# Performance work log

Measured on AMD Instinct MI355X. Metric: run time of the kernel, lower is better.

The kernel has to match this reference:

```python
import jax, jax.numpy as jnp
import numpy as np

B, S, D, H = 4, 2048, 512, 8
HD = D // H  # head dim = 64


def setup_inputs() -> dict:
    key = jax.random.key(0)
    ks = jax.random.split(key, 7)
    s = 0.02
    return {
        "X": jax.random.normal(ks[0], (B, S, D), dtype=jnp.float32),
        "Y": jax.random.normal(ks[1], (B, S, D), dtype=jnp.float32),
        "Z": jax.random.normal(ks[2], (B, S, D), dtype=jnp.float32),
        # weights stored as [in, out] (torch Linear weight transposed)
        "Wq": jax.random.normal(ks[3], (D, D), dtype=jnp.float32) * s,
        "Wk": jax.random.normal(ks[4], (D, D), dtype=jnp.float32) * s,
        "Wv": jax.random.normal(ks[5], (D, D), dtype=jnp.float32) * s,  # dead in original forward
        "Wo": jax.random.normal(ks[6], (D, D), dtype=jnp.float32) * s,
    }


def _split_heads(t):
    # [B, S, D] -> [B, H, S, HD]
    return t.reshape(B, S, H, HD).transpose(0, 2, 1, 3)


def reference(X, Y, Z, Wq, Wk, Wv, Wo):
    q = _split_heads(X @ Wq)
    k = _split_heads(Y @ Wk)
    # NOTE: original module (faithfully) uses W_o for the value projection; W_v is unused.
    v = _split_heads(Z @ Wo)
    scores = jnp.einsum("bhqd,bhkd->bhqk", q, k) / jnp.sqrt(jnp.float32(HD))
    # sigmoid(s) > 0.5  <=>  s > 0 (sigmoid strictly monotone); keep score else 0
    scores = jnp.where(scores > 0, scores, jnp.float32(0))
    attn = jax.nn.softmax(scores, axis=-1)
    out = jnp.einsum("bhqk,bhkd->bhqd", attn, v)  # dropout inactive at eval
    out = out.transpose(0, 2, 1, 3).reshape(B, S, D)  # merge heads
    return out @ Wo
```

## Files before the change

kernel.cpp:

```cpp
#include <hip/hip_runtime.h>
#include <math.h>

#define S_LEN 2048
#define DIM   512
#define M_TOT 8192
#define NCH   (S_LEN / 64)

typedef __attribute__((ext_vector_type(8))) short bf16x8;
typedef __attribute__((ext_vector_type(4))) short bf16x4;
typedef __attribute__((ext_vector_type(4))) float f32x4;
typedef __attribute__((ext_vector_type(16))) float f32x16;

#define MFMA(a, b, c)   __builtin_amdgcn_mfma_f32_16x16x32_bf16((a), (b), (c), 0, 0, 0)
#define MFMA32(a, b, c) __builtin_amdgcn_mfma_f32_32x32x16_bf16((a), (b), (c), 0, 0, 0)

#define QSCALE 0.18033688011112042f

__device__ __forceinline__ short f2b(float x) {
    union { float f; unsigned u; } v; v.f = x;
    unsigned r = v.u + 0x7FFFu + ((v.u >> 16) & 1u);
    return (short)(r >> 16);
}

__device__ __forceinline__ unsigned cvtpk(float a, float b) {
    unsigned r;
    asm("v_cvt_pk_bf16_f32 %0, %1, %2" : "=v"(r) : "v"(a), "v"(b));
    return r;
}

__device__ __forceinline__ bf16x8 cvt8(float4 lo, float4 hi) {
    union { unsigned u[4]; bf16x8 v; } o;
    o.u[0] = cvtpk(lo.x, lo.y);
    o.u[1] = cvtpk(lo.z, lo.w);
    o.u[2] = cvtpk(hi.x, hi.y);
    o.u[3] = cvtpk(hi.z, hi.w);
    return o.v;
}

__device__ __forceinline__ float fast_exp2(float x) {
#if __has_builtin(__builtin_amdgcn_exp2f)
    return __builtin_amdgcn_exp2f(x);
#else
    return __expf(x * 0.693147180559945f);
#endif
}

__global__ __launch_bounds__(256) void prep_wt(const float* Wq, const float* Wk, const float* Wo,
                                               short* Wtq, short* Wtk, short* Wto) {
    const int zi = blockIdx.z;
    const float* W = zi == 0 ? Wq : zi == 1 ? Wk : Wo;
    short*      Wt = zi == 0 ? Wtq : zi == 1 ? Wtk : Wto;
    const float sc = zi == 0 ? QSCALE : 1.0f;
    __shared__ short Ts[64 * 72];
    const int t = threadIdx.x;
    const int k0 = blockIdx.x * 64, n0 = blockIdx.y * 64;
    #pragma unroll
    for (int it = 0; it < 4; ++it) {
        const int r = (t >> 4) + 16 * it;
        const int cq = t & 15;
        float4 v = *(const float4*)&W[(size_t)(k0 + r) * DIM + n0 + cq * 4];
        Ts[(4 * cq + 0) * 72 + r] = f2b(v.x * sc);
        Ts[(4 * cq + 1) * 72 + r] = f2b(v.y * sc);
        Ts[(4 * cq + 2) * 72 + r] = f2b(v.z * sc);
        Ts[(4 * cq + 3) * 72 + r] = f2b(v.w * sc);
    }
    __syncthreads();
    #pragma unroll
    for (int it = 0; it < 2; ++it) {
        const int n = (t >> 3) + 32 * it;
        const int sg = t & 7;
        *(bf16x8*)&Wt[(size_t)(n0 + n) * DIM + k0 + sg * 8] = *(const bf16x8*)&Ts[n * 72 + sg * 8];
    }
}

__global__ __launch_bounds__(256) void proj_gemm(const float* __restrict__ X,
                                                 const float* __restrict__ Y,
                                                 const float* __restrict__ Z,
                                                 const short* __restrict__ Wtq,
                                                 const short* __restrict__ Wtk,
                                                 const short* __restrict__ Wto,
                                                 short* __restrict__ Qb,
                                                 short* __restrict__ Kb,
                                                 short* __restrict__ Vt) {
    const int zi = blockIdx.y;
    const float* A  = zi == 0 ? X : zi == 1 ? Y : Z;
    const short* Bw = zi == 0 ? Wtq : zi == 1 ? Wtk : Wto;

    __shared__ short As[64 * 40];
    __shared__ short Bs[512 * 40];
    const int tid = threadIdx.x;
    const int w = tid >> 6, ln = tid & 63, l15 = ln & 15, quad = ln >> 4;
    const int m0 = blockIdx.x * 64;
    const int wn = w * 128;

    const int r0 = tid >> 2;
    const int sg = tid & 3;
    const float* ap = A + (size_t)(m0 + r0) * DIM + sg * 8;
    const short* bp = Bw + (size_t)r0 * DIM + sg * 8;

    float4 a0l = *(const float4*)ap, a0h = *(const float4*)(ap + 4);
    bf16x8 br[8];
    #pragma unroll
    for (int i = 0; i < 8; ++i)
        br[i] = *(const bf16x8*)(bp + (size_t)(64 * i) * DIM);

    f32x4 acc[4][8] = {};

    for (int k0 = 0; k0 < DIM; k0 += 32) {
        __syncthreads();
        *(bf16x8*)&As[r0 * 40 + sg * 8] = cvt8(a0l, a0h);
        #pragma unroll
        for (int i = 0; i < 8; ++i)
            *(bf16x8*)&Bs[(r0 + 64 * i) * 40 + sg * 8] = br[i];
        __syncthreads();
        const int kn = (k0 + 32 < DIM) ? k0 + 32 : 0;
        a0l = *(const float4*)(ap + kn); a0h = *(const float4*)(ap + kn + 4);
        #pragma unroll
        for (int i = 0; i < 8; ++i)
            br[i] = *(const bf16x8*)(bp + (size_t)(64 * i) * DIM + kn);

        bf16x8 af[4];
        #pragma unroll
        for (int mf = 0; mf < 4; ++mf)
            af[mf] = *(const bf16x8*)&As[(16 * mf + l15) * 40 + quad * 8];
        #pragma unroll
        for (int nf = 0; nf < 8; ++nf) {
            bf16x8 bfr = *(const bf16x8*)&Bs[(wn + 16 * nf + l15) * 40 + quad * 8];
            #pragma unroll
            for (int mf = 0; mf < 4; ++mf)
                acc[mf][nf] = MFMA(af[mf], bfr, acc[mf][nf]);
        }
    }

    if (zi < 2) {
        short* C = zi == 0 ? Qb : Kb;
        #pragma unroll
        for (int mf = 0; mf < 4; ++mf)
            #pragma unroll
            for (int nf = 0; nf < 8; ++nf)
                #pragma unroll
                for (int r = 0; r < 4; ++r)
                    C[(size_t)(m0 + 16 * mf + 4 * quad + r) * DIM + wn + 16 * nf + l15] =
                        f2b(acc[mf][nf][r]);
    } else {
        #pragma unroll
        for (int mf = 0; mf < 4; ++mf)
            #pragma unroll
            for (int nf = 0; nf < 8; ++nf) {
                const int col = wn + 16 * nf + l15;
                const int h = col >> 6, hd = col & 63;
                const int row0_ = m0 + 16 * mf + 4 * quad;
                const int bb = row0_ >> 11, s0 = row0_ & 2047;
                bf16x4 o = { f2b(acc[mf][nf][0]), f2b(acc[mf][nf][1]),
                             f2b(acc[mf][nf][2]), f2b(acc[mf][nf][3]) };
                *(bf16x4*)&Vt[((size_t)((bb * 8 + h) * 64 + hd)) * S_LEN + s0] = o;
            }
    }
}

__global__ __launch_bounds__(256) void out_gemm(const short* __restrict__ Ob,
                                                const short* __restrict__ Wto,
                                                float* __restrict__ Cout) {
    __shared__ short As[64 * 40];
    __shared__ short Bs[64 * 40];
    const int tid = threadIdx.x;
    const int w = tid >> 6, ln = tid & 63, l15 = ln & 15, quad = ln >> 4;

    const int f = blockIdx.x;
    const int swz = ((f & 7) << 7) | (f >> 3);
    const int m0 = (swz >> 3) * 64, n0 = (swz & 7) * 64;
    const int wm = (w & 1) * 32, wn = (w >> 1) * 32;

    const int row = tid >> 2;
    const int sg = tid & 3;
    const short* ap = Ob  + (size_t)(m0 + row) * DIM + sg * 8;
    const short* bp = Wto + (size_t)(n0 + row) * DIM + sg * 8;

    bf16x8 a0 = *(const bf16x8*)ap, b0 = *(const bf16x8*)bp;

    f32x4 acc[2][2] = {};

    for (int k0 = 0; k0 < DIM; k0 += 32) {
        __syncthreads();
        *(bf16x8*)&As[row * 40 + sg * 8] = a0;
        *(bf16x8*)&Bs[row * 40 + sg * 8] = b0;
        __syncthreads();
        const int kn = (k0 + 32 < DIM) ? k0 + 32 : 0;
        a0 = *(const bf16x8*)(ap + kn); b0 = *(const bf16x8*)(bp + kn);

        bf16x8 af[2], bf[2];
        #pragma unroll
        for (int mf = 0; mf < 2; ++mf) af[mf] = *(const bf16x8*)&As[(wm + 16 * mf + l15) * 40 + quad * 8];
        #pragma unroll
        for (int nf = 0; nf < 2; ++nf) bf[nf] = *(const bf16x8*)&Bs[(wn + 16 * nf + l15) * 40 + quad * 8];
        #pragma unroll
        for (int mf = 0; mf < 2; ++mf)
            #pragma unroll
            for (int nf = 0; nf < 2; ++nf)
                acc[mf][nf] = MFMA(af[mf], bf[nf], acc[mf][nf]);
    }
    #pragma unroll
    for (int mf = 0; mf < 2; ++mf)
        #pragma unroll
        for (int nf = 0; nf < 2; ++nf)
            #pragma unroll
            for (int r = 0; r < 4; ++r)
                Cout[(size_t)(m0 + wm + 16 * mf + 4 * quad + r) * DIM + n0 + wn + 16 * nf + l15] =
                    acc[mf][nf][r];
}

__global__ __launch_bounds__(256) void attn_mfma(const short* __restrict__ Qb,
                                                 const short* __restrict__ Kb,
                                                 const short* __restrict__ Vtg,
                                                 short* __restrict__ Ob) {
    __shared__ short Ks[2][64 * 72];
    __shared__ short Vs[2][64 * 72];
    __shared__ float Ds[4][32];

    const int tid = threadIdx.x;
    const int w = tid >> 6, ln = tid & 63, n31 = ln & 31, hL = ln >> 5;

    const int f = blockIdx.x;
    const int swz = ((f & 7) << 6) | (f >> 3);
    const int qt0 = (swz & 15) * 128;
    const int bh  = swz >> 4;
    const int b = bh >> 3, h = bh & 7;
    const size_t tokbase = (size_t)b * S_LEN;

    const int q0w = qt0 + 32 * w;
    bf16x8 qf[4];
    #pragma unroll
    for (int dk = 0; dk < 4; ++dk)
        qf[dk] = *(const bf16x8*)&Qb[(tokbase + q0w + n31) * DIM + h * 64 + 16 * dk + 8 * hL];

    const int srow = tid >> 2, sg = tid & 3;
    const short* kbase = Kb  + (tokbase + srow) * DIM + h * 64 + sg * 16;
    const short* vbase = Vtg + ((size_t)bh * 64 + srow) * S_LEN;

    union b8split { bf16x8 v; struct { bf16x4 lo, hi; } s; };

    bf16x8 kr0, kr1;
    b8split vrA, vrB;

    f32x16 oacc[2] = {};
    f32x4 d4 = {0.f, 0.f, 0.f, 0.f};

    kr0 = *(const bf16x8*)kbase;       kr1 = *(const bf16x8*)(kbase + 8);
    vrA.v = *(const bf16x8*)(vbase + 8 * sg);
    vrB.v = *(const bf16x8*)(vbase + 32 + 8 * sg);
    *(bf16x8*)&Ks[0][srow * 72 + sg * 16]     = kr0;
    *(bf16x8*)&Ks[0][srow * 72 + sg * 16 + 8] = kr1;
    {
        short* vrow = &Vs[0][srow * 72 + 16 * sg];
        *(bf16x4*)&vrow[0]  = vrA.s.lo;  *(bf16x4*)&vrow[8]  = vrA.s.hi;
        *(bf16x4*)&vrow[4]  = vrB.s.lo;  *(bf16x4*)&vrow[12] = vrB.s.hi;
    }
    kr0 = *(const bf16x8*)(kbase + (size_t)64 * DIM);
    kr1 = *(const bf16x8*)(kbase + (size_t)64 * DIM + 8);
    vrA.v = *(const bf16x8*)(vbase + 64 + 8 * sg);
    vrB.v = *(const bf16x8*)(vbase + 64 + 32 + 8 * sg);
    __syncthreads();

    for (int kc = 0; kc < NCH; ++kc) {
        const int cur = kc & 1;
        if (kc + 1 < NCH) {
            *(bf16x8*)&Ks[cur ^ 1][srow * 72 + sg * 16]     = kr0;
            *(bf16x8*)&Ks[cur ^ 1][srow * 72 + sg * 16 + 8] = kr1;
            short* vrow = &Vs[cur ^ 1][srow * 72 + 16 * sg];
            *(bf16x4*)&vrow[0]  = vrA.s.lo;  *(bf16x4*)&vrow[8]  = vrA.s.hi;
            *(bf16x4*)&vrow[4]  = vrB.s.lo;  *(bf16x4*)&vrow[12] = vrB.s.hi;
        }
        if (kc + 2 < NCH) {
            const size_t ko = (size_t)(kc + 2) * 64 * DIM;
            const size_t vo = (size_t)(kc + 2) * 64;
            kr0 = *(const bf16x8*)(kbase + ko);
            kr1 = *(const bf16x8*)(kbase + ko + 8);
            vrA.v = *(const bf16x8*)(vbase + vo + 8 * sg);
            vrB.v = *(const bf16x8*)(vbase + vo + 32 + 8 * sg);
        }

        f32x16 sacc[2] = {};
        __builtin_amdgcn_s_setprio(1);
        #pragma unroll
        for (int kt = 0; kt < 2; ++kt)
            #pragma unroll
            for (int dk = 0; dk < 4; ++dk) {
                bf16x8 ka = *(const bf16x8*)&Ks[cur][(32 * kt + n31) * 72 + 16 * dk + 8 * hL];
                sacc[kt] = MFMA32(ka, qf[dk], sacc[kt]);
            }
        __builtin_amdgcn_s_setprio(0);

        unsigned cp[16];
        #pragma unroll
        for (int kt = 0; kt < 2; ++kt)
            #pragma unroll
            for (int p = 0; p < 8; ++p) {
                const float e0 = fast_exp2(fmaxf(sacc[kt][2 * p], 0.f));
                const float e1 = fast_exp2(fmaxf(sacc[kt][2 * p + 1], 0.f));
                d4[p & 3] += e0 + e1;
                cp[8 * kt + p] = cvtpk(e0, e1);
            }

        __builtin_amdgcn_s_setprio(1);
        #pragma unroll
        for (int m = 0; m < 4; ++m) {
            union { unsigned u[4]; bf16x8 v; } pu;
            pu.u[0] = cp[2 * m];     pu.u[1] = cp[2 * m + 1];
            pu.u[2] = cp[2 * m + 8]; pu.u[3] = cp[2 * m + 9];
            #pragma unroll
            for (int nt = 0; nt < 2; ++nt) {
                bf16x8 vb = *(const bf16x8*)&Vs[cur][(32 * nt + n31) * 72 + 16 * m + 8 * hL];
                oacc[nt] = MFMA32(pu.v, vb, oacc[nt]);
            }
        }
        __builtin_amdgcn_s_setprio(0);
        __syncthreads();
    }

    float dtot = (d4[0] + d4[1]) + (d4[2] + d4[3]);
    dtot += __shfl_xor(dtot, 32);
    const float dinv = 1.0f / dtot;
    if (ln < 32) Ds[w][n31] = dinv;
    __syncthreads();
    f32x4 dv[4];
    #pragma unroll
    for (int g = 0; g < 4; ++g)
        dv[g] = *(const f32x4*)&Ds[w][8 * g + 4 * hL];

    #pragma unroll
    for (int nt = 0; nt < 2; ++nt)
        #pragma unroll
        for (int r = 0; r < 16; ++r) {
            const int qb = 32 * w + 4 * hL + 8 * (r >> 2) + (r & 3);
            Ob[(tokbase + qt0 + qb) * DIM + h * 64 + 32 * nt + n31] =
                f2b(oacc[nt][r] * dv[r >> 2][r & 3]);
        }
}

extern "C" void kernel_launch(void* const* d_in, const int* in_sizes, int n_in,
                              void* d_out, int out_size, void* d_ws, size_t ws_size,
                              hipStream_t stream) {
    const float* X  = (const float*)d_in[0];
    const float* Y  = (const float*)d_in[1];
    const float* Z  = (const float*)d_in[2];
    const float* Wq = (const float*)d_in[3];
    const float* Wk = (const float*)d_in[4];
    const float* Wo = (const float*)d_in[6];

    char* p = (char*)d_ws;
    const size_t MD = (size_t)M_TOT * DIM;
    short* Qb  = (short*)p; p += MD * 2;
    short* Kb  = (short*)p; p += MD * 2;
    short* Vt  = (short*)p; p += MD * 2;
    short* Ob  = (short*)p; p += MD * 2;
    short* Wtq = (short*)p; p += (size_t)DIM * DIM * 2;
    short* Wtk = (short*)p; p += (size_t)DIM * DIM * 2;
    short* Wto = (short*)p; p += (size_t)DIM * DIM * 2;

    prep_wt<<<dim3(8, 8, 3), 256, 0, stream>>>(Wq, Wk, Wo, Wtq, Wtk, Wto);
    proj_gemm<<<dim3(128, 3), 256, 0, stream>>>(X, Y, Z, Wtq, Wtk, Wto, Qb, Kb, Vt);
    attn_mfma<<<dim3(512), 256, 0, stream>>>(Qb, Kb, Vt, Ob);
    out_gemm<<<dim3(1024), 256, 0, stream>>>(Ob, Wto, (float*)d_out);
}
```

Measured before the change: 197.9 us.

## Retile projection GEMM to 64x128 tiles with 32x32 MFMA and swizzled grid

The projection GEMM now gives each block a 64x128 output tile instead of a full 64x512 row panel, which raises the grid from 384 to 1536 blocks and shrinks the B shared-memory tile fourfold. Inner math switches from 16x16x32 to 32x32x16 bf16 MFMA, so each wave owns a 64x32 slice held in two 16-float accumulators. The block index is swizzled so consecutive blocks share N tiles. The aim is better occupancy and CU coverage, at the cost of re-reading and re-converting the fp32 A rows four times and less reuse of A per load.

After: 193.5 us. 1.02x faster.

```diff
diff --git a/kernel.cpp b/kernel.cpp
--- a/kernel.cpp
+++ b/kernel.cpp
@@ -87,72 +87,68 @@
     const short* Bw = zi == 0 ? Wtq : zi == 1 ? Wtk : Wto;
 
     __shared__ short As[64 * 40];
-    __shared__ short Bs[512 * 40];
+    __shared__ short Bs[128 * 40];
     const int tid = threadIdx.x;
-    const int w = tid >> 6, ln = tid & 63, l15 = ln & 15, quad = ln >> 4;
-    const int m0 = blockIdx.x * 64;
-    const int wn = w * 128;
-
-    const int r0 = tid >> 2;
-    const int sg = tid & 3;
-    const float* ap = A + (size_t)(m0 + r0) * DIM + sg * 8;
-    const short* bp = Bw + (size_t)r0 * DIM + sg * 8;
+    const int w = tid >> 6, ln = tid & 63, n31 = ln & 31, hL = ln >> 5;
+
+    const int lin = blockIdx.x;
+    const int j = lin >> 3;
+    const int m0 = (((lin & 7) << 4) + (j >> 2)) * 64;
+    const int n0 = (j & 3) * 128;
+
+    const int row = tid >> 2;
+    const int sgk = (tid & 3) * 8;
+    const float* ap = A  + (size_t)(m0 + row) * DIM + sgk;
+    const short* bp = Bw + (size_t)(n0 + row) * DIM + sgk;
 
     float4 a0l = *(const float4*)ap, a0h = *(const float4*)(ap + 4);
-    bf16x8 br[8];
-    #pragma unroll
-    for (int i = 0; i < 8; ++i)
-        br[i] = *(const bf16x8*)(bp + (size_t)(64 * i) * DIM);
-
-    f32x4 acc[4][8] = {};
+    bf16x8 br0 = *(const bf16x8*)bp;
+    bf16x8 br1 = *(const bf16x8*)(bp + (size_t)64 * DIM);
+
+    f32x16 acc[2] = {};
 
     for (int k0 = 0; k0 < DIM; k0 += 32) {
         __syncthreads();
-        *(bf16x8*)&As[r0 * 40 + sg * 8] = cvt8(a0l, a0h);
-        #pragma unroll
-        for (int i = 0; i < 8; ++i)
-            *(bf16x8*)&Bs[(r0 + 64 * i) * 40 + sg * 8] = br[i];
+        *(bf16x8*)&As[row * 40 + sgk] = cvt8(a0l, a0h);
+        *(bf16x8*)&Bs[row * 40 + sgk] = br0;
+        *(bf16x8*)&Bs[(row + 64) * 40 + sgk] = br1;
         __syncthreads();
         const int kn = (k0 + 32 < DIM) ? k0 + 32 : 0;
         a0l = *(const float4*)(ap + kn); a0h = *(const float4*)(ap + kn + 4);
-        #pragma unroll
-        for (int i = 0; i < 8; ++i)
-            br[i] = *(const bf16x8*)(bp + (size_t)(64 * i) * DIM + kn);
-
-        bf16x8 af[4];
-        #pragma unroll
-        for (int mf = 0; mf < 4; ++mf)
-            af[mf] = *(const bf16x8*)&As[(16 * mf + l15) * 40 + quad * 8];
-        #pragma unroll
-        for (int nf = 0; nf < 8; ++nf) {
-            bf16x8 bfr = *(const bf16x8*)&Bs[(wn + 16 * nf + l15) * 40 + quad * 8];
-            #pragma unroll
-            for (int mf = 0; mf < 4; ++mf)
-                acc[mf][nf] = MFMA(af[mf], bfr, acc[mf][nf]);
-        }
-    }
-
+        br0 = *(const bf16x8*)(bp + kn);
+        br1 = *(const bf16x8*)(bp + (size_t)64 * DIM + kn);
+
+        #pragma unroll
+        for (int dk = 0; dk < 2; ++dk) {
+            bf16x8 bf = *(const bf16x8*)&Bs[(32 * w + n31) * 40 + 16 * dk + 8 * hL];
+            #pragma unroll
+            for (int mf = 0; mf < 2; ++mf) {
+                bf16x8 af = *(const bf16x8*)&As[(32 * mf + n31) * 40 + 16 * dk + 8 * hL];
+                acc[mf] = MFMA32(af, bf, acc[mf]);
+            }
+        }
+    }
+
+    const int col = n0 + 32 * w + n31;
     if (zi < 2) {
         short* C = zi == 0 ? Qb : Kb;
         #pragma unroll
-        for (int mf = 0; mf < 4; ++mf)
-            #pragma unroll
-            for (int nf = 0; nf < 8; ++nf)
-                #pragma unroll
-                for (int r = 0; r < 4; ++r)
-                    C[(size_t)(m0 + 16 * mf + 4 * quad + r) * DIM + wn + 16 * nf + l15] =
-                        f2b(acc[mf][nf][r]);
+        for (int mf = 0; mf < 2; ++mf)
+            #pragma unroll
+            for (int r = 0; r < 16; ++r) {
+                const int rowo = m0 + 32 * mf + (r & 3) + 8 * (r >> 2) + 4 * hL;
+                C[(size_t)rowo * DIM + col] = f2b(acc[mf][r]);
+            }
     } else {
-        #pragma unroll
-        for (int mf = 0; mf < 4; ++mf)
-            #pragma unroll
-            for (int nf = 0; nf < 8; ++nf) {
-                const int col = wn + 16 * nf + l15;
-                const int h = col >> 6, hd = col & 63;
-                const int row0_ = m0 + 16 * mf + 4 * quad;
+        const int h = col >> 6, hd = col & 63;
+        #pragma unroll
+        for (int mf = 0; mf < 2; ++mf)
+            #pragma unroll
+            for (int rr = 0; rr < 4; ++rr) {
+                const int row0_ = m0 + 32 * mf + 8 * rr + 4 * hL;
                 const int bb = row0_ >> 11, s0 = row0_ & 2047;
-                bf16x4 o = { f2b(acc[mf][nf][0]), f2b(acc[mf][nf][1]),
-                             f2b(acc[mf][nf][2]), f2b(acc[mf][nf][3]) };
+                bf16x4 o = { f2b(acc[mf][4 * rr + 0]), f2b(acc[mf][4 * rr + 1]),
+                             f2b(acc[mf][4 * rr + 2]), f2b(acc[mf][4 * rr + 3]) };
                 *(bf16x4*)&Vt[((size_t)((bb * 8 + h) * 64 + hd)) * S_LEN + s0] = o;
             }
     }
@@ -358,7 +354,7 @@
     short* Wto = (short*)p; p += (size_t)DIM * DIM * 2;
 
     prep_wt<<<dim3(8, 8, 3), 256, 0, stream>>>(Wq, Wk, Wo, Wtq, Wtk, Wto);
-    proj_gemm<<<dim3(128, 3), 256, 0, stream>>>(X, Y, Z, Wtq, Wtk, Wto, Qb, Kb, Vt);
+    proj_gemm<<<dim3(512, 3), 256, 0, stream>>>(X, Y, Z, Wtq, Wtk, Wto, Qb, Kb, Vt);
     attn_mfma<<<dim3(512), 256, 0, stream>>>(Qb, Kb, Vt, Ob);
     out_gemm<<<dim3(1024), 256, 0, stream>>>(Ob, Wto, (float*)d_out);
 }
```
